# Optimization experiments

Measured on AMD Instinct MI355X. Metric: run time of the kernel, lower is better.

The kernel has to match this reference:

```python
import jax, jax.numpy as jnp
import numpy as np

BETA = 5.0
B, D, K, E2 = 64, 3072, 512, 64


def setup_inputs() -> dict:
    key = jax.random.key(0)
    k1, k2, k3, k4 = jax.random.split(key, 4)
    images = jax.random.normal(k1, (B, D), dtype=jnp.float32)
    w_proj = jax.random.normal(k2, (K, D), dtype=jnp.float32) * 0.02   # project.weight
    w_img2 = jax.random.normal(k3, (K, D * E2), dtype=jnp.float32) * 0.02  # img2.weight
    w_rec = jax.random.normal(k4, (E2, K), dtype=jnp.float32) * 0.02   # rec.weight
    return {"images": images, "w_proj": w_proj, "w_img2": w_img2, "w_rec": w_rec}


def reference(images, w_proj, w_img2, w_rec):
    beta = BETA
    wimg = w_proj.T            # (D, K)
    wrec = w_rec.T             # (K, E2)
    # img2.weight (K, D*E2) -> codebook tensor (K, D, E2), std-normalized over D (ddof=1 to match torch)
    wimg2 = w_img2.reshape(K, D, E2)
    wimg2 = wimg2 / (0.01 + jnp.std(wimg2, axis=1, keepdims=True, ddof=1))

    # ---- encode ----
    xd = images[:, :, None] - wimg[None]          # (B, D, K)
    xh = -jnp.mean(xd * xd, axis=1) * beta        # (B, K)
    xp = jax.nn.softmax(xh, axis=-1)              # (B, K)
    lat1 = xp @ wrec                              # (B, E2)
    xe = jnp.einsum('bdk,kde->bke', xd, wimg2)    # (B, K, E2)
    lat2 = jnp.einsum('bke,bk->be', xe, xp)       # (B, E2)

    # ---- decode ----
    diff = lat1[:, :, None] - wrec.T[None]        # (B, E2, K); wrec.T is (E2, K)
    xh2 = -jnp.mean(diff * diff, axis=1) * beta   # (B, K)
    xp2 = jax.nn.softmax(xh2, axis=-1)            # (B, K)
    xx = xp2[:, :, None] * lat2[:, None, :]       # (B, K, E2)
    xd2 = jnp.einsum('bke,kde->bd', xx, wimg2)    # (B, D)
    images_recon = xp2 @ wimg.T + xd2             # (B, D)

    loss = jnp.mean((images_recon - images) ** 2, axis=-1)  # (B,)
    return loss
```

## Files before the change

### kernel.cpp

```cpp
#include <hip/hip_runtime.h>
#include <math.h>

#define Bn 64
#define Dn 3072
#define Kn 512
#define En 64

static constexpr float BETA = 5.0f;

static constexpr size_t ZF_OFF    = 0;
static constexpr size_t ACCP_OFF  = 1048576;
static constexpr size_t PART_OFF  = 1048576;
static constexpr size_t STATP_OFF = 5242880;
static constexpr size_t S_OFF     = 5439488;
static constexpr size_t PACC_OFF  = 5472256;
static constexpr size_t DOTP_OFF  = 5505024;
static constexpr size_t NPROJ_OFF = 5570560;
static constexpr size_t XP2B_OFF  = 5571072;
static constexpr size_t WRECT_OFF = 5587456;
static constexpr size_t FRAG_OFF  = 5620224;

typedef float  f4  __attribute__((ext_vector_type(4)));
typedef __bf16 bf8 __attribute__((ext_vector_type(8)));
typedef int    i4  __attribute__((ext_vector_type(4)));

union AB { i4 i; bf8 b; };

__device__ __forceinline__ unsigned short bf16b(float x) {
  __bf16 h = (__bf16)x;
  union Cv { __bf16 h; unsigned short u; } c;
  c.h = h;
  return c.u;
}

__device__ __forceinline__ float waveAllMax(float v) {
#pragma unroll
  for (int o = 32; o; o >>= 1) v = fmaxf(v, __shfl_xor(v, o));
  return v;
}
__device__ __forceinline__ float waveAllSum(float v) {
#pragma unroll
  for (int o = 32; o; o >>= 1) v += __shfl_xor(v, o);
  return v;
}

__global__ __launch_bounds__(256) void kPT(const float* __restrict__ img,
                                           const float* __restrict__ wrec,
                                           float* __restrict__ ws) {
  const int t = threadIdx.x;
  if (blockIdx.x < 96) {
    const int ds = blockIdx.x;
    const int T = t >> 6, l = t & 63;
    const int b = 16 * T + (l & 15);
    const int d0 = 32 * ds + 8 * (l >> 4);
    const float* p = img + (size_t)b * Dn + d0;
    unsigned short u[8];
#pragma unroll
    for (int j = 0; j < 8; ++j) u[j] = bf16b(p[j]);
    i4 v;
    v.x = (int)u[0] | ((int)u[1] << 16);
    v.y = (int)u[2] | ((int)u[3] << 16);
    v.z = (int)u[4] | ((int)u[5] << 16);
    v.w = (int)u[6] | ((int)u[7] << 16);
    ((i4*)(ws + FRAG_OFF))[(ds * 4 + T) * 64 + l] = v;
  } else {
    int g = (blockIdx.x - 96) * 256 + t;
    int k = g >> 6, e = g & 63;
    ws[WRECT_OFF + g] = wrec[(size_t)e * Kn + k];
  }
}

__global__ __launch_bounds__(256, 4) void kA(const float* __restrict__ wproj,
                                             const float* __restrict__ w2,
                                             float* __restrict__ ws) {
  const int k = blockIdx.x, h = blockIdx.y, t = threadIdx.x;
  const int w = t >> 6, l = t & 63, elane = l & 15, dgrp = l >> 4;
  const int ecol = 16 * w + elane;
  const int n0 = h * 48;
  __shared__ float wp[Dn / 2];
  __shared__ __bf16 wpb[Dn / 2];
  const float* wpk = wproj + (size_t)k * Dn + (size_t)h * (Dn / 2);
  if (t < 192) {
    f4 x = ((const f4*)wpk)[2 * t];
    f4 y = ((const f4*)wpk)[2 * t + 1];
    ((f4*)wp)[2 * t] = x;
    ((f4*)wp)[2 * t + 1] = y;
    i4 v;
    v.x = (int)bf16b(x.x) | ((int)bf16b(x.y) << 16);
    v.y = (int)bf16b(x.z) | ((int)bf16b(x.w) << 16);
    v.z = (int)bf16b(y.x) | ((int)bf16b(y.y) << 16);
    v.w = (int)bf16b(y.z) | ((int)bf16b(y.w) << 16);
    ((i4*)wpb)[t] = v;
  }
  __syncthreads();

  const i4* afr = (const i4*)(ws + FRAG_OFF);
  const float* w2k = w2 + (size_t)k * (Dn * En);
  f4 acc0 = {0.f,0.f,0.f,0.f}, acc1 = {0.f,0.f,0.f,0.f};
  f4 acc2 = {0.f,0.f,0.f,0.f}, acc3 = {0.f,0.f,0.f,0.f};
  f4 dac0 = {0.f,0.f,0.f,0.f}, dac1 = {0.f,0.f,0.f,0.f};
  f4 dac2 = {0.f,0.f,0.f,0.f}, dac3 = {0.f,0.f,0.f,0.f};
  float ssum = 0.f, ssq = 0.f, pacc = 0.f;
  float bwA[8], bwB[8];
  i4 avA[4], avB[4];
#pragma unroll
  for (int j = 0; j < 8; ++j)
    bwA[j] = w2k[(size_t)(n0 * 32 + 8 * dgrp + j) * 64 + ecol];
#pragma unroll
  for (int T = 0; T < 4; ++T) avA[T] = afr[((size_t)n0 * 4 + T) * 64 + l];

#define KA_STEP(BWC, BWN, AVC, AVN, NL) {                                        \
    const int nl1 = (NL) + 1;                                                    \
    if (nl1 < 48) {                                                              \
      _Pragma("unroll")                                                          \
      for (int j = 0; j < 8; ++j)                                                \
        BWN[j] = w2k[(size_t)((n0 + nl1) * 32 + 8 * dgrp + j) * 64 + ecol];      \
      _Pragma("unroll")                                                          \
      for (int T = 0; T < 4; ++T)                                                \
        AVN[T] = afr[((size_t)(n0 + nl1) * 4 + T) * 64 + l];                     \
    }                                                                            \
    bf8 bfr;                                                                     \
    _Pragma("unroll")                                                            \
    for (int j = 0; j < 8; ++j) {                                                \
      float v = BWC[j];                                                          \
      ssum += v; ssq = fmaf(v, v, ssq);                                          \
      pacc = fmaf(wp[(NL) * 32 + 8 * dgrp + j], v, pacc);                        \
      bfr[j] = (__bf16)v;                                                        \
    }                                                                            \
    bf8 wfr = *(const bf8*)&wpb[(NL) * 32 + 8 * dgrp];                           \
    AB a0, a1, a2, a3;                                                           \
    a0.i = AVC[0]; a1.i = AVC[1]; a2.i = AVC[2]; a3.i = AVC[3];                  \
    acc0 = __builtin_amdgcn_mfma_f32_16x16x32_bf16(a0.b, bfr, acc0, 0, 0, 0);    \
    acc1 = __builtin_amdgcn_mfma_f32_16x16x32_bf16(a1.b, bfr, acc1, 0, 0, 0);    \
    acc2 = __builtin_amdgcn_mfma_f32_16x16x32_bf16(a2.b, bfr, acc2, 0, 0, 0);    \
    acc3 = __builtin_amdgcn_mfma_f32_16x16x32_bf16(a3.b, bfr, acc3, 0, 0, 0);    \
    dac0 = __builtin_amdgcn_mfma_f32_16x16x32_bf16(a0.b, wfr, dac0, 0, 0, 0);    \
    dac1 = __builtin_amdgcn_mfma_f32_16x16x32_bf16(a1.b, wfr, dac1, 0, 0, 0);    \
    dac2 = __builtin_amdgcn_mfma_f32_16x16x32_bf16(a2.b, wfr, dac2, 0, 0, 0);    \
    dac3 = __builtin_amdgcn_mfma_f32_16x16x32_bf16(a3.b, wfr, dac3, 0, 0, 0);    \
  }

  for (int nl = 0; nl < 48; nl += 2) {
    KA_STEP(bwA, bwB, avA, avB, nl)
    KA_STEP(bwB, bwA, avB, avA, nl + 1)
  }
#undef KA_STEP

  ssum += __shfl_xor(ssum, 16); ssum += __shfl_xor(ssum, 32);
  ssq  += __shfl_xor(ssq, 16);  ssq  += __shfl_xor(ssq, 32);
  pacc += __shfl_xor(pacc, 16); pacc += __shfl_xor(pacc, 32);
  const size_t kh = (size_t)(k * 2 + h);
  if (dgrp == 0) {
    ws[STATP_OFF + kh * 192 + 0 * 64 + ecol] = ssum;
    ws[STATP_OFF + kh * 192 + 1 * 64 + ecol] = ssq;
    ws[STATP_OFF + kh * 192 + 2 * 64 + ecol] = pacc;
  }
  if (w == 0 && elane == 0) {
#pragma unroll
    for (int T = 0; T < 4; ++T) {
      f4 d = (T == 0) ? dac0 : (T == 1) ? dac1 : (T == 2) ? dac2 : dac3;
#pragma unroll
      for (int r = 0; r < 4; ++r) {
        int b = 16 * T + 4 * dgrp + r;
        ws[DOTP_OFF + (size_t)h * (Bn * Kn) + (size_t)b * Kn + k] = d[r];
      }
    }
  }
#pragma unroll
  for (int T = 0; T < 4; ++T) {
    f4 a = (T == 0) ? acc0 : (T == 1) ? acc1 : (T == 2) ? acc2 : acc3;
#pragma unroll
    for (int r = 0; r < 4; ++r) {
      int b = 16 * T + 4 * dgrp + r;
      ws[ACCP_OFF + kh * 4096 + (size_t)b * 64 + ecol] = a[r];
    }
  }
}

__global__ __launch_bounds__(64) void kStat(const float* __restrict__ wproj,
                                            float* __restrict__ ws) {
  const int k = blockIdx.x, e = threadIdx.x;
  const size_t o0 = STATP_OFF + (size_t)(2 * k) * 192;
  const size_t o1 = STATP_OFF + (size_t)(2 * k + 1) * 192;
  float ssum = ws[o0 + e] + ws[o1 + e];
  float ssq  = ws[o0 + 64 + e] + ws[o1 + 64 + e];
  float pacc = ws[o0 + 128 + e] + ws[o1 + 128 + e];
  float var = (ssq - ssum * ssum * (1.0f / Dn)) * (1.0f / (Dn - 1));
  float sv = 1.0f / (0.01f + sqrtf(fmaxf(var, 0.f)));
  ws[S_OFF + (size_t)k * 64 + e] = sv;
  ws[PACC_OFF + (size_t)k * 64 + e] = pacc;
  float np = 0.f;
  const float* wr = wproj + (size_t)k * Dn;
#pragma unroll 8
  for (int i = 0; i < 48; ++i) {
    float v = wr[i * 64 + e];
    np = fmaf(v, v, np);
  }
  np = waveAllSum(np);
  if (e == 0) ws[NPROJ_OFF + k] = np;
}

__global__ __launch_bounds__(256) void kMid(const float* __restrict__ img,
                                            float* __restrict__ ws) {
  const int b = blockIdx.x;
  const int t = threadIdx.x;
  const int wid = t >> 6, lane = t & 63;
  __shared__ float xp_sh[512];
  __shared__ float red[16];
  __shared__ __align__(16) float scratch[1024];
  __shared__ __align__(16) float l1_sh[64];
  __shared__ float l2_sh[64];

  float acc = 0.f;
  const f4* irow = (const f4*)(img + (size_t)b * Dn);
#pragma unroll
  for (int i = 0; i < 3; ++i) {
    f4 v = irow[t + 256 * i];
    acc = fmaf(v.x, v.x, acc); acc = fmaf(v.y, v.y, acc);
    acc = fmaf(v.z, v.z, acc); acc = fmaf(v.w, v.w, acc);
  }
  acc = waveAllSum(acc);
  if (lane == 0) red[wid] = acc;
  __syncthreads();
  const float nimg = red[0] + red[1] + red[2] + red[3];

  float d1 = ws[DOTP_OFF + (size_t)b * Kn + t]
           + ws[DOTP_OFF + (size_t)(Bn * Kn) + (size_t)b * Kn + t];
  float d2 = ws[DOTP_OFF + (size_t)b * Kn + t + 256]
           + ws[DOTP_OFF + (size_t)(Bn * Kn) + (size_t)b * Kn + t + 256];
  float np1 = ws[NPROJ_OFF + t];
  float np2 = ws[NPROJ_OFF + t + 256];
  const float c = -(BETA / Dn);
  float x1 = c * (nimg - 2.f * d1 + np1);
  float x2 = c * (nimg - 2.f * d2 + np2);

  float m = waveAllMax(fmaxf(x1, x2));
  if (lane == 0) red[4 + wid] = m;
  __syncthreads();
  m = fmaxf(fmaxf(red[4], red[5]), fmaxf(red[6], red[7]));
  float e1 = expf(x1 - m), e2 = expf(x2 - m);
  float sv = waveAllSum(e1 + e2);
  if (lane == 0) red[8 + wid] = sv;
  __syncthreads();
  float inv = 1.f / (red[8] + red[9] + red[10] + red[11]);
  xp_sh[t] = e1 * inv;
  xp_sh[t + 256] = e2 * inv;
  __syncthreads();

  const int eq = t & 15, kq = t >> 4;
  const int k0 = kq * 32;
  const f4* wrect4 = (const f4*)(ws + WRECT_OFF);
  f4 l1v = {0.f, 0.f, 0.f, 0.f};
#pragma unroll 4
  for (int i = 0; i < 32; ++i) {
    int k = k0 + i;
    l1v += xp_sh[k] * wrect4[k * 16 + eq];
  }
  ((f4*)scratch)[kq * 16 + eq] = l1v;
  __syncthreads();
  if (t < 64) {
    float s = 0.f;
#pragma unroll
    for (int q = 0; q < 16; ++q) s += scratch[q * 64 + t];
    l1_sh[t] = s;
  }
  __syncthreads();

  const f4* accp4 = (const f4*)(ws + ACCP_OFF);
  const f4* s4 = (const f4*)(ws + S_OFF);
  const f4* pc4 = (const f4*)(ws + PACC_OFF);
  f4 l2v = {0.f, 0.f, 0.f, 0.f};
#pragma unroll 4
  for (int i = 0; i < 32; ++i) {
    int k = k0 + i;
    f4 a0 = accp4[(size_t)(2 * k) * 1024 + b * 16 + eq];
    f4 a1 = accp4[(size_t)(2 * k + 1) * 1024 + b * 16 + eq];
    f4 svv = s4[k * 16 + eq];
    f4 pcc = pc4[k * 16 + eq];
    l2v += (xp_sh[k] * svv) * ((a0 + a1) - pcc);
  }
  __syncthreads();
  ((f4*)scratch)[kq * 16 + eq] = l2v;
  __syncthreads();
  if (t < 64) {
    float s = 0.f;
#pragma unroll
    for (int q = 0; q < 16; ++q) s += scratch[q * 64 + t];
    l2_sh[t] = s;
  }

  float h1 = 0.f, h2 = 0.f;
#pragma unroll
  for (int i = 0; i < 16; ++i) {
    f4 lv = *(const f4*)&l1_sh[i * 4];
    f4 w1 = *(const f4*)&ws[WRECT_OFF + (size_t)t * En + i * 4];
    f4 w2v = *(const f4*)&ws[WRECT_OFF + ((size_t)t + 256) * En + i * 4];
    float a0 = lv.x - w1.x, a1 = lv.y - w1.y, a2 = lv.z - w1.z, a3 = lv.w - w1.w;
    h1 = fmaf(a0, a0, h1); h1 = fmaf(a1, a1, h1);
    h1 = fmaf(a2, a2, h1); h1 = fmaf(a3, a3, h1);
    float b0 = lv.x - w2v.x, b1 = lv.y - w2v.y, b2 = lv.z - w2v.z, b3 = lv.w - w2v.w;
    h2 = fmaf(b0, b0, h2); h2 = fmaf(b1, b1, h2);
    h2 = fmaf(b2, b2, h2); h2 = fmaf(b3, b3, h2);
  }
  const float c2 = -(BETA / En);
  x1 = c2 * h1; x2 = c2 * h2;

  m = waveAllMax(fmaxf(x1, x2));
  if (lane == 0) red[4 + wid] = m;
  __syncthreads();
  m = fmaxf(fmaxf(red[4], red[5]), fmaxf(red[6], red[7]));
  e1 = expf(x1 - m); e2 = expf(x2 - m);
  sv = waveAllSum(e1 + e2);
  if (lane == 0) red[8 + wid] = sv;
  __syncthreads();
  inv = 1.f / (red[8] + red[9] + red[10] + red[11]);
  float p1 = e1 * inv, p2 = e2 * inv;
  unsigned short* xpb = (unsigned short*)(ws + XP2B_OFF);
  xpb[(size_t)b * Kn + t] = bf16b(p1);
  xpb[(size_t)b * Kn + t + 256] = bf16b(p2);

  const int T = b >> 4, bl = b & 15;
  i4* zf = (i4*)(ws + ZF_OFF);
#pragma unroll
  for (int kk = 0; kk < 2; ++kk) {
    const int k = t + 256 * kk;
    const float p = kk ? p2 : p1;
#pragma unroll
    for (int g = 0; g < 8; ++g) {
      const int dgrp = g & 3;
      const int S = 2 * k + (g >> 2);
      const int l = dgrp * 16 + bl;
      unsigned short u[8];
#pragma unroll
      for (int j = 0; j < 8; ++j) {
        int e = 8 * g + j;
        u[j] = bf16b(p * l2_sh[e] * ws[S_OFF + (size_t)k * En + e]);
      }
      i4 v;
      v.x = (int)u[0] | ((int)u[1] << 16);
      v.y = (int)u[2] | ((int)u[3] << 16);
      v.z = (int)u[4] | ((int)u[5] << 16);
      v.w = (int)u[6] | ((int)u[7] << 16);
      zf[((size_t)S * 4 + T) * 64 + l] = v;
    }
  }
}

__global__ __launch_bounds__(256, 3) void kB(const float* __restrict__ wproj,
                                             const float* __restrict__ w2,
                                             float* __restrict__ ws) {
  const int dtile = blockIdx.x, ks = blockIdx.y, t = threadIdx.x;
  const int w = t >> 6, l = t & 63, elane = l & 15, dgrp = l >> 4;
  const int d = dtile * 64 + 16 * w + elane;
  const i4* zfr = (const i4*)(ws + ZF_OFF);
  f4 acc0 = {0.f,0.f,0.f,0.f}, acc1 = {0.f,0.f,0.f,0.f};
  f4 acc2 = {0.f,0.f,0.f,0.f}, acc3 = {0.f,0.f,0.f,0.f};
  f4 bwA[2], bwB[2];
  i4 avA[4], avB[4];
  {
    const f4* p = (const f4*)(w2 + ((size_t)(ks * 32) * Dn + d) * En + 8 * dgrp);
    bwA[0] = p[0]; bwA[1] = p[1];
#pragma unroll
    for (int T = 0; T < 4; ++T) avA[T] = zfr[((size_t)(ks * 64) * 4 + T) * 64 + l];
  }

#define KB_ITER(BWC, BWN, AVC, AVN, N) {                                         \
    const int np1 = (N) + 1;                                                     \
    if (np1 < 64) {                                                              \
      const int kk = ks * 32 + (np1 >> 1);                                       \
      const int e0 = (np1 & 1) * 32;                                             \
      const f4* p = (const f4*)(w2 + ((size_t)kk * Dn + d) * En + e0 + 8 * dgrp);\
      BWN[0] = p[0]; BWN[1] = p[1];                                              \
      _Pragma("unroll")                                                          \
      for (int T = 0; T < 4; ++T)                                                \
        AVN[T] = zfr[((size_t)(ks * 64 + np1) * 4 + T) * 64 + l];                \
    }                                                                            \
    bf8 bfr;                                                                     \
    _Pragma("unroll")                                                            \
    for (int j = 0; j < 4; ++j) {                                                \
      bfr[j] = (__bf16)BWC[0][j];                                                \
      bfr[4 + j] = (__bf16)BWC[1][j];                                            \
    }                                                                            \
    AB a0, a1, a2, a3;                                                           \
    a0.i = AVC[0]; a1.i = AVC[1]; a2.i = AVC[2]; a3.i = AVC[3];                  \
    acc0 = __builtin_amdgcn_mfma_f32_16x16x32_bf16(a0.b, bfr, acc0, 0, 0, 0);    \
    acc1 = __builtin_amdgcn_mfma_f32_16x16x32_bf16(a1.b, bfr, acc1, 0, 0, 0);    \
    acc2 = __builtin_amdgcn_mfma_f32_16x16x32_bf16(a2.b, bfr, acc2, 0, 0, 0);    \
    acc3 = __builtin_amdgcn_mfma_f32_16x16x32_bf16(a3.b, bfr, acc3, 0, 0, 0);    \
  }

  for (int n = 0; n < 64; n += 2) {
    KB_ITER(bwA, bwB, avA, avB, n)
    KB_ITER(bwB, bwA, avB, avA, n + 1)
  }
#undef KB_ITER

  {
    const int kk0 = ks * 32;
    bf8 bw;
#pragma unroll
    for (int j = 0; j < 8; ++j)
      bw[j] = (__bf16)wproj[(size_t)(kk0 + 8 * dgrp + j) * Dn + d];
    const unsigned short* xpb = (const unsigned short*)(ws + XP2B_OFF);
    AB a0, a1, a2, a3;
    a0.i = *(const i4*)&xpb[(size_t)(0 * 16 + elane) * Kn + kk0 + 8 * dgrp];
    a1.i = *(const i4*)&xpb[(size_t)(1 * 16 + elane) * Kn + kk0 + 8 * dgrp];
    a2.i = *(const i4*)&xpb[(size_t)(2 * 16 + elane) * Kn + kk0 + 8 * dgrp];
    a3.i = *(const i4*)&xpb[(size_t)(3 * 16 + elane) * Kn + kk0 + 8 * dgrp];
    acc0 = __builtin_amdgcn_mfma_f32_16x16x32_bf16(a0.b, bw, acc0, 0, 0, 0);
    acc1 = __builtin_amdgcn_mfma_f32_16x16x32_bf16(a1.b, bw, acc1, 0, 0, 0);
    acc2 = __builtin_amdgcn_mfma_f32_16x16x32_bf16(a2.b, bw, acc2, 0, 0, 0);
    acc3 = __builtin_amdgcn_mfma_f32_16x16x32_bf16(a3.b, bw, acc3, 0, 0, 0);
  }

#pragma unroll
  for (int T = 0; T < 4; ++T) {
    f4 a = (T == 0) ? acc0 : (T == 1) ? acc1 : (T == 2) ? acc2 : acc3;
#pragma unroll
    for (int r = 0; r < 4; ++r) {
      int b = 16 * T + 4 * dgrp + r;
      ws[PART_OFF + ((size_t)ks * Bn + b) * Dn + d] = a[r];
    }
  }
}

__global__ __launch_bounds__(256) void kLoss(const float* __restrict__ img,
                                             const float* __restrict__ ws,
                                             float* __restrict__ out) {
  const int b = blockIdx.x, t = threadIdx.x;
  __shared__ float red[4];
  float acc = 0.f;
  const f4* p4 = (const f4*)(ws + PART_OFF);
  const f4* i4p = (const f4*)(img + (size_t)b * Dn);
  const int rowq = Dn / 4;
#pragma unroll
  for (int i = 0; i < 3; ++i) {
    int idx = t + 256 * i;
    f4 r = {0.f, 0.f, 0.f, 0.f};
#pragma unroll
    for (int s = 0; s < 16; ++s)
      r += p4[((size_t)s * Bn + b) * rowq + idx];
    f4 v = i4p[idx];
    float dx = r.x - v.x, dy = r.y - v.y, dz = r.z - v.z, dw = r.w - v.w;
    acc = fmaf(dx, dx, acc); acc = fmaf(dy, dy, acc);
    acc = fmaf(dz, dz, acc); acc = fmaf(dw, dw, acc);
  }
  acc = waveAllSum(acc);
  if ((t & 63) == 0) red[t >> 6] = acc;
  __syncthreads();
  if (t == 0) out[b] = (red[0] + red[1] + red[2] + red[3]) * (1.0f / Dn);
}

extern "C" void kernel_launch(void* const* d_in, const int* in_sizes, int n_in,
                              void* d_out, int out_size, void* d_ws, size_t ws_size,
                              hipStream_t stream) {
  const float* img   = (const float*)d_in[0];
  const float* wproj = (const float*)d_in[1];
  const float* w2    = (const float*)d_in[2];
  const float* wrec  = (const float*)d_in[3];
  float* ws  = (float*)d_ws;
  float* out = (float*)d_out;

  hipLaunchKernelGGL(kPT,   dim3(224), dim3(256), 0, stream, img, wrec, ws);
  hipLaunchKernelGGL(kA,    dim3(512, 2), dim3(256), 0, stream, wproj, w2, ws);
  hipLaunchKernelGGL(kStat, dim3(512), dim3(64), 0, stream, wproj, ws);
  hipLaunchKernelGGL(kMid,  dim3(64),  dim3(256), 0, stream, img, ws);
  hipLaunchKernelGGL(kB,    dim3(48, 16), dim3(256), 0, stream, wproj, w2, ws);
  hipLaunchKernelGGL(kLoss, dim3(64),  dim3(256), 0, stream, img, ws, out);
}
```

Measured before the change: 248.4 us.

## Stage bf16 copy of img2 weights in kA for kB to read

kA already converts each fp32 codebook value to bf16 for its MFMAs. It now also stores those bf16 values to a new workspace region. kB then loads the bf16 copy directly instead of reloading and converting the full fp32 tensor, which halves kB's read traffic and drops its conversion instructions. In exchange, kA writes roughly 200MB of narrow, partly scattered 2-byte stores, so total memory traffic stays about the same, and the workspace must be large enough for the extra buffer.

```diff
diff --git a/kernel.cpp b/kernel.cpp
--- a/kernel.cpp
+++ b/kernel.cpp
@@ -19,6 +19,7 @@
 static constexpr size_t XP2B_OFF  = 5571072;
 static constexpr size_t WRECT_OFF = 5587456;
 static constexpr size_t FRAG_OFF  = 5620224;
+static constexpr size_t W2B_OFF   = 5718528;
 
 typedef float  f4  __attribute__((ext_vector_type(4)));
 typedef __bf16 bf8 __attribute__((ext_vector_type(8)));
@@ -96,6 +97,7 @@
 
   const i4* afr = (const i4*)(ws + FRAG_OFF);
   const float* w2k = w2 + (size_t)k * (Dn * En);
+  __bf16* w2bk = (__bf16*)(ws + W2B_OFF) + (size_t)k * (Dn * En);
   f4 acc0 = {0.f,0.f,0.f,0.f}, acc1 = {0.f,0.f,0.f,0.f};
   f4 acc2 = {0.f,0.f,0.f,0.f}, acc3 = {0.f,0.f,0.f,0.f};
   f4 dac0 = {0.f,0.f,0.f,0.f}, dac1 = {0.f,0.f,0.f,0.f};
@@ -127,6 +129,9 @@
       pacc = fmaf(wp[(NL) * 32 + 8 * dgrp + j], v, pacc);                        \
       bfr[j] = (__bf16)v;                                                        \
     }                                                                            \
+    _Pragma("unroll")                                                            \
+    for (int j = 0; j < 8; ++j)                                                  \
+      w2bk[(size_t)((n0 + (NL)) * 32 + 8 * dgrp + j) * 64 + ecol] = bfr[j];      \
     bf8 wfr = *(const bf8*)&wpb[(NL) * 32 + 8 * dgrp];                           \
     AB a0, a1, a2, a3;                                                           \
     a0.i = AVC[0]; a1.i = AVC[1]; a2.i = AVC[2]; a3.i = AVC[3];                  \
@@ -347,19 +352,18 @@
 }
 
 __global__ __launch_bounds__(256, 3) void kB(const float* __restrict__ wproj,
-                                             const float* __restrict__ w2,
                                              float* __restrict__ ws) {
   const int dtile = blockIdx.x, ks = blockIdx.y, t = threadIdx.x;
   const int w = t >> 6, l = t & 63, elane = l & 15, dgrp = l >> 4;
   const int d = dtile * 64 + 16 * w + elane;
   const i4* zfr = (const i4*)(ws + ZF_OFF);
+  const unsigned short* w2b = (const unsigned short*)(ws + W2B_OFF);
   f4 acc0 = {0.f,0.f,0.f,0.f}, acc1 = {0.f,0.f,0.f,0.f};
   f4 acc2 = {0.f,0.f,0.f,0.f}, acc3 = {0.f,0.f,0.f,0.f};
-  f4 bwA[2], bwB[2];
+  i4 bwA, bwB;
   i4 avA[4], avB[4];
   {
-    const f4* p = (const f4*)(w2 + ((size_t)(ks * 32) * Dn + d) * En + 8 * dgrp);
-    bwA[0] = p[0]; bwA[1] = p[1];
+    bwA = *(const i4*)(w2b + ((size_t)(ks * 32) * Dn + d) * En + 8 * dgrp);
 #pragma unroll
     for (int T = 0; T < 4; ++T) avA[T] = zfr[((size_t)(ks * 64) * 4 + T) * 64 + l];
   }
@@ -369,24 +373,18 @@
     if (np1 < 64) {                                                              \
       const int kk = ks * 32 + (np1 >> 1);                                       \
       const int e0 = (np1 & 1) * 32;                                             \
-      const f4* p = (const f4*)(w2 + ((size_t)kk * Dn + d) * En + e0 + 8 * dgrp);\
-      BWN[0] = p[0]; BWN[1] = p[1];                                              \
+      BWN = *(const i4*)(w2b + ((size_t)kk * Dn + d) * En + e0 + 8 * dgrp);      \
       _Pragma("unroll")                                                          \
       for (int T = 0; T < 4; ++T)                                                \
         AVN[T] = zfr[((size_t)(ks * 64 + np1) * 4 + T) * 64 + l];                \
     }                                                                            \
-    bf8 bfr;                                                                     \
-    _Pragma("unroll")                                                            \
-    for (int j = 0; j < 4; ++j) {                                                \
-      bfr[j] = (__bf16)BWC[0][j];                                                \
-      bfr[4 + j] = (__bf16)BWC[1][j];                                            \
-    }                                                                            \
+    AB bb; bb.i = BWC;                                                           \
     AB a0, a1, a2, a3;                                                           \
     a0.i = AVC[0]; a1.i = AVC[1]; a2.i = AVC[2]; a3.i = AVC[3];                  \
-    acc0 = __builtin_amdgcn_mfma_f32_16x16x32_bf16(a0.b, bfr, acc0, 0, 0, 0);    \
-    acc1 = __builtin_amdgcn_mfma_f32_16x16x32_bf16(a1.b, bfr, acc1, 0, 0, 0);    \
-    acc2 = __builtin_amdgcn_mfma_f32_16x16x32_bf16(a2.b, bfr, acc2, 0, 0, 0);    \
-    acc3 = __builtin_amdgcn_mfma_f32_16x16x32_bf16(a3.b, bfr, acc3, 0, 0, 0);    \
+    acc0 = __builtin_amdgcn_mfma_f32_16x16x32_bf16(a0.b, bb.b, acc0, 0, 0, 0);   \
+    acc1 = __builtin_amdgcn_mfma_f32_16x16x32_bf16(a1.b, bb.b, acc1, 0, 0, 0);   \
+    acc2 = __builtin_amdgcn_mfma_f32_16x16x32_bf16(a2.b, bb.b, acc2, 0, 0, 0);   \
+    acc3 = __builtin_amdgcn_mfma_f32_16x16x32_bf16(a3.b, bb.b, acc3, 0, 0, 0);   \
   }
 
   for (int n = 0; n < 64; n += 2) {
@@ -465,6 +463,6 @@
   hipLaunchKernelGGL(kA,    dim3(512, 2), dim3(256), 0, stream, wproj, w2, ws);
   hipLaunchKernelGGL(kStat, dim3(512), dim3(64), 0, stream, wproj, ws);
   hipLaunchKernelGGL(kMid,  dim3(64),  dim3(256), 0, stream, img, ws);
-  hipLaunchKernelGGL(kB,    dim3(48, 16), dim3(256), 0, stream, wproj, w2, ws);
+  hipLaunchKernelGGL(kB,    dim3(48, 16), dim3(256), 0, stream, wproj, ws);
   hipLaunchKernelGGL(kLoss, dim3(64),  dim3(256), 0, stream, img, ws, out);
 }
```

Result: slower. 463.9 us (+86.8%).
